# Performance work log

Measured on AMD Instinct MI355X. Metric: run time of the kernel, lower is better.

Reference implementation:

```python
import jax, jax.numpy as jnp
import numpy as np

N = 50000   # nodes
E = 800000  # edges
IN, H, O, C = 128, 256, 256, 64
G = 64      # graphs in batch


def setup_inputs() -> dict:
    key = jax.random.key(0)
    ks = jax.random.split(key, 10)
    x = jax.random.normal(ks[0], (N, IN), dtype=jnp.float32)
    edge_index = jax.random.randint(ks[1], (2, E), 0, N, dtype=jnp.int32)
    batch = jnp.sort(jax.random.randint(ks[2], (N,), 0, G, dtype=jnp.int32))
    # learned params (PyG GCNConv: weight [in, out] + bias [out]; nn.Linear)
    W1 = jax.random.normal(ks[3], (IN, H), dtype=jnp.float32) / np.sqrt(IN)
    b1 = jnp.zeros((H,), dtype=jnp.float32)
    W2 = jax.random.normal(ks[4], (H, O), dtype=jnp.float32) / np.sqrt(H)
    b2 = jnp.zeros((O,), dtype=jnp.float32)
    Wfc = jax.random.normal(ks[5], (O, C), dtype=jnp.float32) / np.sqrt(O)
    bfc = jnp.zeros((C,), dtype=jnp.float32)
    return {"x": x, "edge_index": edge_index, "batch": batch,
            "W1": W1, "b1": b1, "W2": W2, "b2": b2, "Wfc": Wfc, "bfc": bfc}


def reference(x, edge_index, batch, W1, b1, W2, b2, Wfc, bfc):
    src, dst = edge_index[0], edge_index[1]
    # degree with self-loops (PyG GCNConv default: add_self_loops=True, sym norm)
    deg = jax.ops.segment_sum(jnp.ones((E,), x.dtype), dst, num_segments=N) + 1.0
    dinv = jax.lax.rsqrt(deg)                      # D^{-1/2}
    edge_norm = (dinv[src] * dinv[dst])[:, None]   # [E, 1]
    self_norm = (dinv * dinv)[:, None]             # [N, 1] self-loop weight

    def gcn_conv(h, W, b):
        h = h @ W                                  # transform first (PyG order)
        agg = jax.ops.segment_sum(h[src] * edge_norm, dst, num_segments=N)
        return agg + h * self_norm + b

    h = jax.nn.gelu(gcn_conv(x, W1, b1), approximate=False)  # nn.GELU exact
    h = gcn_conv(h, W2, b2)

    # global_mean_pool over graph ids
    cnt = jax.ops.segment_sum(jnp.ones((N,), h.dtype), batch, num_segments=G)
    pooled = jax.ops.segment_sum(h, batch, num_segments=G) / jnp.maximum(cnt, 1.0)[:, None]
    return pooled @ Wfc + bfc                      # [G, C]
```

## Files before the change

### kernel.cpp

```cpp
#include <hip/hip_runtime.h>
#include <hip/hip_bf16.h>
#include <hip/hip_fp16.h>
#include <math.h>

#define NNODES 50000
#define NEDGES 800000
#define FIN 128
#define FH 256
#define NG 64
#define NC 64
#define SCAN_NB ((NNODES + 255) / 256)
#define NP 50176
#define QSK 196
#define DEG_BLOCKS ((NEDGES + 255) / 256)
#define SPLITX_ITEMS (NNODES * FIN / 4)
#define SPLITX_BLOCKS ((SPLITX_ITEMS + 255) / 256)
#define GEMM_MB ((NNODES + 127) / 128)
#define GEMM_BLKS (GEMM_MB * 2)
#define QTR (NP / 4)

#define NBUCK 196
#define BCAP 5120
#define BIN_CHUNK 4096
#define BIN_BLOCKS ((NEDGES + BIN_CHUNK - 1) / BIN_CHUNK)

typedef unsigned short bhalf;
typedef __attribute__((ext_vector_type(8))) short bf16x8;
typedef __attribute__((ext_vector_type(4))) float f32x4;
typedef __attribute__((ext_vector_type(4))) unsigned short u16x4;

__device__ inline bhalf f2bf_rn(float f) {
    unsigned int u = __float_as_uint(f);
    u += 0x7FFFu + ((u >> 16) & 1u);
    return (bhalf)(u >> 16);
}
__device__ inline float bf2f(bhalf h) { return __uint_as_float(((unsigned int)h) << 16); }
__device__ inline float2 bfpair(unsigned int u) {
    return make_float2(__uint_as_float(u << 16), __uint_as_float(u & 0xFFFF0000u));
}


__global__ void degree_splitx_kernel(const int* __restrict__ dst, int* __restrict__ degi,
                                     const float* __restrict__ x, bhalf* __restrict__ xb) {
    int b = blockIdx.x;
    if (b < DEG_BLOCKS) {
        int e = b * 256 + threadIdx.x;
        if (e < NEDGES) atomicAdd(&degi[dst[e]], 1);
    } else {
        int i = (b - DEG_BLOCKS) * 256 + threadIdx.x;
        if (i < SPLITX_ITEMS) {
            float4 v = *reinterpret_cast<const float4*>(&x[i * 4]);
            u16x4 o = {f2bf_rn(v.x), f2bf_rn(v.y), f2bf_rn(v.z), f2bf_rn(v.w)};
            *reinterpret_cast<u16x4*>(&xb[i * 4]) = o;
        }
    }
}


__global__ __launch_bounds__(256)
void scan_block_kernel(const int* __restrict__ degi, int* __restrict__ local_ex,
                       int* __restrict__ partial, float* __restrict__ dinv, int Nn) {
    __shared__ int s[256];
    int i = blockIdx.x * 256 + threadIdx.x;
    int v = (i < Nn) ? degi[i] : 0;
    s[threadIdx.x] = v;
    __syncthreads();
#pragma unroll
    for (int off = 1; off < 256; off <<= 1) {
        int t = (threadIdx.x >= off) ? s[threadIdx.x - off] : 0;
        __syncthreads();
        s[threadIdx.x] += t;
        __syncthreads();
    }
    if (i < Nn) {
        local_ex[i] = s[threadIdx.x] - v;
        dinv[i] = rsqrtf((float)v + 1.0f);
    }
    if (threadIdx.x == 255) partial[blockIdx.x] = s[255];
}


__global__ __launch_bounds__(256)
void add_offsets_kernel(int* __restrict__ row_start, const int* __restrict__ local_ex,
                        const int* __restrict__ partial, int* __restrict__ bcur,
                        const float* __restrict__ W1, bhalf* __restrict__ w1t, int Nn) {
    __shared__ int s[256];
    int t = threadIdx.x;
    s[t] = (t < blockIdx.x) ? partial[t] : 0;
    __syncthreads();
#pragma unroll
    for (int off = 128; off > 0; off >>= 1) {
        if (t < off) s[t] += s[t + off];
        __syncthreads();
    }
    int prefix = s[0];
    int i = blockIdx.x * 256 + t;
    if (i < Nn) row_start[i] = local_ex[i] + prefix;
    if (blockIdx.x == 0 && t < NBUCK) bcur[t] = t * BCAP;
    if (i < FIN * 256) {
        int k = i >> 8, n = i & 255;
        w1t[n * FIN + k] = f2bf_rn(W1[i]);
    }
}


__global__ __launch_bounds__(256)
void bin_kernel(const int* __restrict__ src, const int* __restrict__ dst,
                const float* __restrict__ dinv, int* __restrict__ bcur,
                uint2* __restrict__ binned) {
    __shared__ int hist[NBUCK];
    __shared__ int base[NBUCK];
    __shared__ int gb[NBUCK];
    __shared__ int lcur[NBUCK];
    __shared__ int scan_tmp[256];
    __shared__ uint2 stage[BIN_CHUNK];
    __shared__ unsigned char bid[BIN_CHUNK];
    int t = threadIdx.x;
    int e0 = blockIdx.x * BIN_CHUNK;
    for (int i = t; i < NBUCK; i += 256) hist[i] = 0;
    __syncthreads();
#pragma unroll
    for (int k = 0; k < BIN_CHUNK / 256; k++) {
        int e = e0 + k * 256 + t;
        if (e < NEDGES) atomicAdd(&hist[dst[e] >> 8], 1);
    }
    __syncthreads();
    int v = (t < NBUCK) ? hist[t] : 0;
    scan_tmp[t] = v;
    __syncthreads();
#pragma unroll
    for (int off = 1; off < 256; off <<= 1) {
        int x = (t >= off) ? scan_tmp[t - off] : 0;
        __syncthreads();
        scan_tmp[t] += x;
        __syncthreads();
    }
    if (t < NBUCK) {
        int ex = scan_tmp[t] - v;
        base[t] = ex;
        lcur[t] = ex;
        gb[t] = (v > 0) ? atomicAdd(&bcur[t], v) : 0;
    }
    __syncthreads();
#pragma unroll
    for (int k = 0; k < BIN_CHUNK / 256; k++) {
        int e = e0 + k * 256 + t;
        if (e < NEDGES) {
            int s = src[e], d = dst[e];
            int b = d >> 8;
            float nm = dinv[s] * dinv[d];
            int lp = atomicAdd(&lcur[b], 1);
            stage[lp] = make_uint2((unsigned int)s | ((unsigned int)(d & 255) << 17),
                                   __float_as_uint(nm));
            bid[lp] = (unsigned char)b;
        }
    }
    __syncthreads();
    int total = base[NBUCK - 1] + hist[NBUCK - 1];
    for (int i = t; i < total; i += 256) {
        int b = bid[i];
        binned[(size_t)gb[b] + (i - base[b])] = stage[i];
    }
}


__global__ __launch_bounds__(256)
void place_kernel(const uint2* __restrict__ binned, const int* __restrict__ bcur,
                  const int* __restrict__ row_start, uint2* __restrict__ edata) {
    __shared__ int lcur[256];
    int b = blockIdx.x;
    int t = threadIdx.x;
    lcur[t] = 0;
    __syncthreads();
    int cnt = bcur[b] - b * BCAP;
    int nb0 = b << 8;
    const uint2* bp = &binned[(size_t)b * BCAP];
    for (int i = t; i < cnt; i += 256) {
        uint2 e = bp[i];
        int dl = (e.x >> 17) & 255;
        int pos = row_start[nb0 + dl] + atomicAdd(&lcur[dl], 1);
        edata[pos] = make_uint2(e.x & 0x1FFFFu, e.y);
    }
}


__global__ __launch_bounds__(256)
void gather128_kernel(const bhalf* __restrict__ xb, const uint2* __restrict__ edata,
                      const int* __restrict__ row_start, const int* __restrict__ degi,
                      const float* __restrict__ dinv, bhalf* __restrict__ z, int Nn) {
    int node = blockIdx.x * 4 + (threadIdx.x >> 6);
    if (node >= Nn) return;
    int lane = threadIdx.x & 63;
    int st = row_start[node];
    int cnt = degi[node];
    float ax = 0.0f, ay = 0.0f;
    int j = 0;
    for (; j + 3 < cnt; j += 4) {
        uint2 e0 = edata[st + j],     e1 = edata[st + j + 1];
        uint2 e2 = edata[st + j + 2], e3 = edata[st + j + 3];
        float2 v0 = bfpair(*reinterpret_cast<const unsigned int*>(&xb[(size_t)e0.x * FIN + lane * 2]));
        float2 v1 = bfpair(*reinterpret_cast<const unsigned int*>(&xb[(size_t)e1.x * FIN + lane * 2]));
        float2 v2 = bfpair(*reinterpret_cast<const unsigned int*>(&xb[(size_t)e2.x * FIN + lane * 2]));
        float2 v3 = bfpair(*reinterpret_cast<const unsigned int*>(&xb[(size_t)e3.x * FIN + lane * 2]));
        float n0 = __uint_as_float(e0.y), n1 = __uint_as_float(e1.y);
        float n2 = __uint_as_float(e2.y), n3 = __uint_as_float(e3.y);
        ax += v0.x * n0 + v1.x * n1 + v2.x * n2 + v3.x * n3;
        ay += v0.y * n0 + v1.y * n1 + v2.y * n2 + v3.y * n3;
    }
    for (; j < cnt; j++) {
        uint2 e0 = edata[st + j];
        float2 v0 = bfpair(*reinterpret_cast<const unsigned int*>(&xb[(size_t)e0.x * FIN + lane * 2]));
        float n0 = __uint_as_float(e0.y);
        ax += v0.x * n0; ay += v0.y * n0;
    }
    float sn = dinv[node];
    sn *= sn;
    float2 xv = bfpair(*reinterpret_cast<const unsigned int*>(&xb[(size_t)node * FIN + lane * 2]));
    ushort2 o = {f2bf_rn(ax + xv.x * sn), f2bf_rn(ay + xv.y * sn)};
    *reinterpret_cast<ushort2*>(&z[(size_t)node * FIN + lane * 2]) = o;
}


__global__ __launch_bounds__(256)
void wt_build_kernel(const uint2* __restrict__ edata, const int* __restrict__ row_start,
                     const int* __restrict__ batch, const float* __restrict__ dinv,
                     bhalf* __restrict__ wthi, bhalf* __restrict__ wtlo) {
    __shared__ float acc[QTR];
    int g = blockIdx.x >> 2;
    int q = blockIdx.x & 3;
    int base = q * QTR;
    for (int i = threadIdx.x; i < QTR; i += 256) acc[i] = 0.0f;
    int lo = 0, hi = NNODES;
    while (lo < hi) { int m = (lo + hi) >> 1; if (batch[m] < g) lo = m + 1; else hi = m; }
    int na = lo;
    hi = NNODES;
    while (lo < hi) { int m = (lo + hi) >> 1; if (batch[m] < g + 1) lo = m + 1; else hi = m; }
    int nb = lo;
    int pa = (na < NNODES) ? row_start[na] : NEDGES;
    int pb = (nb < NNODES) ? row_start[nb] : NEDGES;
    __syncthreads();
    for (int p = pa + threadIdx.x; p < pb; p += 256) {
        uint2 e = edata[p];
        int s = (int)e.x - base;
        if ((unsigned int)s < (unsigned int)QTR)
            atomicAdd(&acc[s], __uint_as_float(e.y));
    }
    __syncthreads();
    size_t rowo = (size_t)g * NP + base;
    for (int i = threadIdx.x; i < QTR; i += 256) {
        int s = base + i;
        float v = acc[i];
        if (s >= na && s < nb) { float dv = dinv[s]; v += dv * dv; }
        bhalf hb = f2bf_rn(v);
        wthi[rowo + i] = hb;
        wtlo[rowo + i] = f2bf_rn(v - bf2f(hb));
    }
}


__global__ __launch_bounds__(256)
void gemm_kernel(const bhalf* __restrict__ A, const bhalf* __restrict__ Bt,
                 const float* __restrict__ bias, bhalf* __restrict__ h1t, int M, int Kp) {
    __shared__ bhalf As[128 * 72];
    __shared__ bhalf Bs[128 * 72];
    const int tid  = threadIdx.x;
    const int lane = tid & 63;
    const int wave = tid >> 6;
    const int quad = lane >> 4;
    const int l15  = lane & 15;
    const int wm = (wave & 1) * 64;
    const int wn = (wave >> 1) * 64;
    const int bm = (blockIdx.x >> 1) * 128;
    const int bn = (blockIdx.x & 1) * 128;

    f32x4 acc[4][4] = {};

    for (int k0 = 0; k0 < Kp; k0 += 64) {
#pragma unroll
        for (int i = 0; i < 4; i++) {
            int chunk = tid + i * 256;
            int r = chunk >> 3, c16 = chunk & 7;
            int gm = bm + r;
            float4 va = make_float4(0.f, 0.f, 0.f, 0.f);
            if (gm < M) va = *reinterpret_cast<const float4*>(&A[(size_t)gm * Kp + k0 + c16 * 8]);
            *reinterpret_cast<float4*>(&As[r * 72 + c16 * 8]) = va;
            float4 vb = *reinterpret_cast<const float4*>(&Bt[(size_t)(bn + r) * Kp + k0 + c16 * 8]);
            *reinterpret_cast<float4*>(&Bs[r * 72 + c16 * 8]) = vb;
        }
        __syncthreads();
#pragma unroll
        for (int kk = 0; kk < 64; kk += 32) {
            bf16x8 af[4], bfr[4];
#pragma unroll
            for (int mi = 0; mi < 4; mi++)
                af[mi] = *reinterpret_cast<const bf16x8*>(&As[(wm + mi * 16 + l15) * 72 + kk + quad * 8]);
#pragma unroll
            for (int ni = 0; ni < 4; ni++)
                bfr[ni] = *reinterpret_cast<const bf16x8*>(&Bs[(wn + ni * 16 + l15) * 72 + kk + quad * 8]);
#pragma unroll
            for (int mi = 0; mi < 4; mi++)
#pragma unroll
                for (int ni = 0; ni < 4; ni++)
                    acc[mi][ni] = __builtin_amdgcn_mfma_f32_16x16x32_bf16(af[mi], bfr[ni], acc[mi][ni], 0, 0, 0);
        }
        __syncthreads();
    }

#pragma unroll
    for (int mi = 0; mi < 4; mi++) {
        int row0 = bm + wm + mi * 16 + quad * 4;
#pragma unroll
        for (int ni = 0; ni < 4; ni++) {
            int col = bn + wn + ni * 16 + l15;
            float bv = bias[col];
            u16x4 o;
#pragma unroll
            for (int r = 0; r < 4; r++) {
                float v = acc[mi][ni][r] + bv;
                v = 0.5f * v * (1.0f + erff(v * 0.70710678118654752f));
                o[r] = f2bf_rn(v);
            }
            *reinterpret_cast<u16x4*>(&h1t[(size_t)col * NP + row0]) = o;
        }
    }
}


__global__ __launch_bounds__(256)
void qsum_mfma_kernel(const bhalf* __restrict__ h1t, const bhalf* __restrict__ wthi,
                      const bhalf* __restrict__ wtlo, float* __restrict__ qpart) {
    const int tid  = threadIdx.x;
    const int lane = tid & 63;
    const int wave = tid >> 6;
    const int quad = lane >> 4;
    const int l15  = lane & 15;
    const int m0 = wave * 64;
    const size_t kbase = (size_t)blockIdx.x * 256 + quad * 8;
    f32x4 acc[4][4] = {};
#pragma unroll
    for (int ks = 0; ks < 8; ks++) {
        size_t k0 = kbase + ks * 32;
        bf16x8 af[4], bh[4], bl[4];
#pragma unroll
        for (int mi = 0; mi < 4; mi++)
            af[mi] = *reinterpret_cast<const bf16x8*>(&h1t[(size_t)(m0 + mi * 16 + l15) * NP + k0]);
#pragma unroll
        for (int ni = 0; ni < 4; ni++) {
            bh[ni] = *reinterpret_cast<const bf16x8*>(&wthi[(size_t)(ni * 16 + l15) * NP + k0]);
            bl[ni] = *reinterpret_cast<const bf16x8*>(&wtlo[(size_t)(ni * 16 + l15) * NP + k0]);
        }
#pragma unroll
        for (int mi = 0; mi < 4; mi++)
#pragma unroll
            for (int ni = 0; ni < 4; ni++) {
                acc[mi][ni] = __builtin_amdgcn_mfma_f32_16x16x32_bf16(af[mi], bh[ni], acc[mi][ni], 0, 0, 0);
                acc[mi][ni] = __builtin_amdgcn_mfma_f32_16x16x32_bf16(af[mi], bl[ni], acc[mi][ni], 0, 0, 0);
            }
    }
    float* qp = &qpart[(size_t)blockIdx.x * NG * FH];
#pragma unroll
    for (int mi = 0; mi < 4; mi++) {
        int row0 = m0 + mi * 16 + quad * 4;
#pragma unroll
        for (int ni = 0; ni < 4; ni++) {
            int col = ni * 16 + l15;
            f32x4 o = {acc[mi][ni][0], acc[mi][ni][1], acc[mi][ni][2], acc[mi][ni][3]};
            *reinterpret_cast<f32x4*>(&qp[(size_t)col * FH + row0]) = o;
        }
    }
}


__global__ __launch_bounds__(256)
void p2fc_kernel(const float* __restrict__ qpart, const float* __restrict__ W2,
                 const float* __restrict__ b2, const int* __restrict__ batch,
                 const float* __restrict__ Wfc, const float* __restrict__ bfc,
                 float* __restrict__ out) {
    __shared__ float qg[FH];
    __shared__ float ps[FH];
    int g = blockIdx.x;
    int t = threadIdx.x;
    float s = 0.0f;
    for (int b = 0; b < QSK; b++)
        s += qpart[(size_t)b * NG * FH + (size_t)g * FH + t];
    qg[t] = s;
    int lo = 0, hi = NNODES;
    while (lo < hi) { int m = (lo + hi) >> 1; if (batch[m] < g) lo = m + 1; else hi = m; }
    int a = lo;
    lo = 0; hi = NNODES;
    while (lo < hi) { int m = (lo + hi) >> 1; if (batch[m] < g + 1) lo = m + 1; else hi = m; }
    float inv = 1.0f / fmaxf((float)(lo - a), 1.0f);
    __syncthreads();
    float acc = 0.0f;
    for (int k = 0; k < FH; k++)
        acc += qg[k] * W2[k * FH + t];
    ps[t] = acc * inv + b2[t];
    __syncthreads();
    if (t < NC) {
        float a2 = 0.0f;
        for (int cc = 0; cc < FH; cc++)
            a2 += ps[cc] * Wfc[cc * NC + t];
        out[g * NC + t] = a2 + bfc[t];
    }
}


extern "C" void kernel_launch(void* const* d_in, const int* in_sizes, int n_in,
                              void* d_out, int out_size, void* d_ws, size_t ws_size,
                              hipStream_t stream) {
    const float* x    = (const float*)d_in[0];
    const int*   ei   = (const int*)d_in[1];
    const int*   batch= (const int*)d_in[2];
    const float* W1   = (const float*)d_in[3];
    const float* b1   = (const float*)d_in[4];
    const float* W2   = (const float*)d_in[5];
    const float* b2   = (const float*)d_in[6];
    const float* Wfc  = (const float*)d_in[7];
    const float* bfc  = (const float*)d_in[8];
    float* out = (float*)d_out;

    const int* src = ei;
    const int* dst = ei + NEDGES;

    bhalf* xb        = (bhalf*)d_ws;
    bhalf* zb        = xb + (size_t)NNODES * FIN;
    bhalf* h1t       = zb + (size_t)NNODES * FIN;
    uint2* edata     = (uint2*)(h1t + (size_t)FH * NP);
    uint2* binned    = edata + NEDGES;
    int*   row_start = (int*)(binned + (size_t)NBUCK * BCAP);
    int*   local_ex  = row_start + NNODES;
    int*   partial   = local_ex + NNODES;
    int*   bcur      = partial + 256;
    float* dinv      = (float*)(bcur + 256);
    bhalf* w1t       = (bhalf*)(dinv + NNODES);
    bhalf* wthi      = w1t + 256 * FIN;
    bhalf* wtlo      = wthi + (size_t)NG * NP;
    float* qpart     = (float*)(wtlo + (size_t)NG * NP);
    int*   degi      = (int*)(qpart + (size_t)QSK * NG * FH);

    (void)hipMemsetAsync(degi, 0, (size_t)NNODES * 4, stream);

    degree_splitx_kernel<<<DEG_BLOCKS + SPLITX_BLOCKS, 256, 0, stream>>>(dst, degi, x, xb);
    scan_block_kernel<<<SCAN_NB, 256, 0, stream>>>(degi, local_ex, partial, dinv, NNODES);
    add_offsets_kernel<<<SCAN_NB, 256, 0, stream>>>(row_start, local_ex, partial, bcur,
                                                    W1, w1t, NNODES);
    bin_kernel<<<BIN_BLOCKS, 256, 0, stream>>>(src, dst, dinv, bcur, binned);
    place_kernel<<<NBUCK, 256, 0, stream>>>(binned, bcur, row_start, edata);

    gather128_kernel<<<(NNODES + 3) / 4, 256, 0, stream>>>(xb, edata, row_start, degi,
                                                           dinv, zb, NNODES);
    wt_build_kernel<<<NG * 4, 256, 0, stream>>>(edata, row_start, batch, dinv, wthi, wtlo);
    gemm_kernel<<<GEMM_BLKS, 256, 0, stream>>>(zb, w1t, b1, h1t, NNODES, FIN);

    qsum_mfma_kernel<<<QSK, 256, 0, stream>>>(h1t, wthi, wtlo, qpart);
    p2fc_kernel<<<NG, FH, 0, stream>>>(qpart, W2, b2, batch, Wfc, bfc, out);
}
```

Measured before the change: 294.5 us.

## Fold degree counting and CSR scan into bucket placement with packed 32-bit edges

Removes the separate atomic degree pass, the two scan kernels and the memset. Each place block now derives per-node degrees, dinv and row offsets from its binned bucket, working in shared memory. Edges are packed into 32 bits: a 16-bit source index plus a half-precision dinv of the destination, replacing the 8-byte (src, float norm) pairs. The gather factors the normalization as dinv[dst]*(sum dinv[src]*x + dinv[dst]*x), reading dinv per source. This cuts launches and edge bandwidth. It relies on node indices fitting in 16 bits, which fails for N=50000 > 65535? No, 50000 fits. It also introduces fp16 rounding of the norm weights in wt_build.

```diff
diff --git a/kernel.cpp b/kernel.cpp
--- a/kernel.cpp
+++ b/kernel.cpp
@@ -9,19 +9,18 @@
 #define FH 256
 #define NG 64
 #define NC 64
-#define SCAN_NB ((NNODES + 255) / 256)
 #define NP 50176
 #define QSK 196
-#define DEG_BLOCKS ((NEDGES + 255) / 256)
 #define SPLITX_ITEMS (NNODES * FIN / 4)
 #define SPLITX_BLOCKS ((SPLITX_ITEMS + 255) / 256)
+#define W1T_BLOCKS (FIN * 256 / 256)
 #define GEMM_MB ((NNODES + 127) / 128)
 #define GEMM_BLKS (GEMM_MB * 2)
 #define QTR (NP / 4)
 
 #define NBUCK 196
 #define BCAP 5120
-#define BIN_CHUNK 4096
+#define BIN_CHUNK 2048
 #define BIN_BLOCKS ((NEDGES + BIN_CHUNK - 1) / BIN_CHUNK)
 
 typedef unsigned short bhalf;
@@ -40,80 +39,36 @@
 }
 
 
-__global__ void degree_splitx_kernel(const int* __restrict__ dst, int* __restrict__ degi,
-                                     const float* __restrict__ x, bhalf* __restrict__ xb) {
+__global__ void splitx_kernel(const float* __restrict__ x, bhalf* __restrict__ xb,
+                              const float* __restrict__ W1, bhalf* __restrict__ w1t,
+                              int* __restrict__ bcur) {
     int b = blockIdx.x;
-    if (b < DEG_BLOCKS) {
-        int e = b * 256 + threadIdx.x;
-        if (e < NEDGES) atomicAdd(&degi[dst[e]], 1);
-    } else {
-        int i = (b - DEG_BLOCKS) * 256 + threadIdx.x;
+    if (b < SPLITX_BLOCKS) {
+        int i = b * 256 + threadIdx.x;
         if (i < SPLITX_ITEMS) {
             float4 v = *reinterpret_cast<const float4*>(&x[i * 4]);
             u16x4 o = {f2bf_rn(v.x), f2bf_rn(v.y), f2bf_rn(v.z), f2bf_rn(v.w)};
             *reinterpret_cast<u16x4*>(&xb[i * 4]) = o;
         }
-    }
-}
-
-
-__global__ __launch_bounds__(256)
-void scan_block_kernel(const int* __restrict__ degi, int* __restrict__ local_ex,
-                       int* __restrict__ partial, float* __restrict__ dinv, int Nn) {
-    __shared__ int s[256];
-    int i = blockIdx.x * 256 + threadIdx.x;
-    int v = (i < Nn) ? degi[i] : 0;
-    s[threadIdx.x] = v;
-    __syncthreads();
-#pragma unroll
-    for (int off = 1; off < 256; off <<= 1) {
-        int t = (threadIdx.x >= off) ? s[threadIdx.x - off] : 0;
-        __syncthreads();
-        s[threadIdx.x] += t;
-        __syncthreads();
-    }
-    if (i < Nn) {
-        local_ex[i] = s[threadIdx.x] - v;
-        dinv[i] = rsqrtf((float)v + 1.0f);
-    }
-    if (threadIdx.x == 255) partial[blockIdx.x] = s[255];
-}
-
-
-__global__ __launch_bounds__(256)
-void add_offsets_kernel(int* __restrict__ row_start, const int* __restrict__ local_ex,
-                        const int* __restrict__ partial, int* __restrict__ bcur,
-                        const float* __restrict__ W1, bhalf* __restrict__ w1t, int Nn) {
-    __shared__ int s[256];
-    int t = threadIdx.x;
-    s[t] = (t < blockIdx.x) ? partial[t] : 0;
-    __syncthreads();
-#pragma unroll
-    for (int off = 128; off > 0; off >>= 1) {
-        if (t < off) s[t] += s[t + off];
-        __syncthreads();
-    }
-    int prefix = s[0];
-    int i = blockIdx.x * 256 + t;
-    if (i < Nn) row_start[i] = local_ex[i] + prefix;
-    if (blockIdx.x == 0 && t < NBUCK) bcur[t] = t * BCAP;
-    if (i < FIN * 256) {
+    } else if (b < SPLITX_BLOCKS + W1T_BLOCKS) {
+        int i = (b - SPLITX_BLOCKS) * 256 + threadIdx.x;
         int k = i >> 8, n = i & 255;
         w1t[n * FIN + k] = f2bf_rn(W1[i]);
+    } else {
+        if (threadIdx.x < NBUCK) bcur[threadIdx.x] = threadIdx.x * BCAP;
     }
 }
 
 
 __global__ __launch_bounds__(256)
 void bin_kernel(const int* __restrict__ src, const int* __restrict__ dst,
-                const float* __restrict__ dinv, int* __restrict__ bcur,
-                uint2* __restrict__ binned) {
+                int* __restrict__ bcur, unsigned int* __restrict__ binned) {
     __shared__ int hist[NBUCK];
     __shared__ int base[NBUCK];
     __shared__ int gb[NBUCK];
     __shared__ int lcur[NBUCK];
     __shared__ int scan_tmp[256];
-    __shared__ uint2 stage[BIN_CHUNK];
+    __shared__ unsigned int stage[BIN_CHUNK];
     __shared__ unsigned char bid[BIN_CHUNK];
     int t = threadIdx.x;
     int e0 = blockIdx.x * BIN_CHUNK;
@@ -148,10 +103,8 @@
         if (e < NEDGES) {
             int s = src[e], d = dst[e];
             int b = d >> 8;
-            float nm = dinv[s] * dinv[d];
             int lp = atomicAdd(&lcur[b], 1);
-            stage[lp] = make_uint2((unsigned int)s | ((unsigned int)(d & 255) << 17),
-                                   __float_as_uint(nm));
+            stage[lp] = (unsigned int)s | ((unsigned int)(d & 255) << 16);
             bid[lp] = (unsigned char)b;
         }
     }
@@ -165,64 +118,103 @@
 
 
 __global__ __launch_bounds__(256)
-void place_kernel(const uint2* __restrict__ binned, const int* __restrict__ bcur,
-                  const int* __restrict__ row_start, uint2* __restrict__ edata) {
+void place_kernel(const unsigned int* __restrict__ binned, const int* __restrict__ bcur,
+                  int* __restrict__ row_start, float* __restrict__ dinv,
+                  unsigned int* __restrict__ edata) {
+    __shared__ unsigned int stage[BCAP];
+    __shared__ int sc[256];
+    __shared__ int deg[256];
+    __shared__ int lex[256];
     __shared__ int lcur[256];
-    int b = blockIdx.x;
-    int t = threadIdx.x;
+    __shared__ unsigned short dih[256];
+    __shared__ int s_ebase, s_cnt;
+    int b = blockIdx.x, t = threadIdx.x;
+    int c = (t < NBUCK) ? (bcur[t] - t * BCAP) : 0;
+    sc[t] = c;
+    __syncthreads();
+#pragma unroll
+    for (int off = 1; off < 256; off <<= 1) {
+        int x = (t >= off) ? sc[t - off] : 0;
+        __syncthreads();
+        sc[t] += x;
+        __syncthreads();
+    }
+    if (t == b) { s_ebase = sc[t] - c; s_cnt = c; }
+    deg[t] = 0;
+    __syncthreads();
+    int cnt = s_cnt, eb = s_ebase;
+    const unsigned int* bp = &binned[(size_t)b * BCAP];
+    for (int i = t; i < cnt; i += 256) stage[i] = bp[i];
+    __syncthreads();
+    for (int i = t; i < cnt; i += 256) atomicAdd(&deg[(stage[i] >> 16) & 255], 1);
+    __syncthreads();
+    int d = deg[t];
+    float di = rsqrtf((float)d + 1.0f);
+    int gn = (b << 8) + t;
+    if (gn < NNODES) dinv[gn] = di;
+    dih[t] = __half_as_ushort(__float2half(di));
+    sc[t] = d;
+    __syncthreads();
+#pragma unroll
+    for (int off = 1; off < 256; off <<= 1) {
+        int x = (t >= off) ? sc[t - off] : 0;
+        __syncthreads();
+        sc[t] += x;
+        __syncthreads();
+    }
+    int lexv = sc[t] - d;
+    lex[t] = lexv;
     lcur[t] = 0;
-    __syncthreads();
-    int cnt = bcur[b] - b * BCAP;
-    int nb0 = b << 8;
-    const uint2* bp = &binned[(size_t)b * BCAP];
+    if (gn <= NNODES) row_start[gn] = eb + lexv;
+    __syncthreads();
     for (int i = t; i < cnt; i += 256) {
-        uint2 e = bp[i];
-        int dl = (e.x >> 17) & 255;
-        int pos = row_start[nb0 + dl] + atomicAdd(&lcur[dl], 1);
-        edata[pos] = make_uint2(e.x & 0x1FFFFu, e.y);
-    }
-}
-
-
-__global__ __launch_bounds__(256)
-void gather128_kernel(const bhalf* __restrict__ xb, const uint2* __restrict__ edata,
-                      const int* __restrict__ row_start, const int* __restrict__ degi,
-                      const float* __restrict__ dinv, bhalf* __restrict__ z, int Nn) {
+        unsigned int e = stage[i];
+        int dl = (e >> 16) & 255;
+        int pos = eb + lex[dl] + atomicAdd(&lcur[dl], 1);
+        edata[pos] = (e & 0xFFFFu) | ((unsigned int)dih[dl] << 16);
+    }
+}
+
+
+__global__ __launch_bounds__(256)
+void gather128_kernel(const bhalf* __restrict__ xb, const unsigned int* __restrict__ edata,
+                      const int* __restrict__ row_start, const float* __restrict__ dinv,
+                      bhalf* __restrict__ z, int Nn) {
     int node = blockIdx.x * 4 + (threadIdx.x >> 6);
     if (node >= Nn) return;
     int lane = threadIdx.x & 63;
     int st = row_start[node];
-    int cnt = degi[node];
+    int cnt = row_start[node + 1] - st;
     float ax = 0.0f, ay = 0.0f;
     int j = 0;
     for (; j + 3 < cnt; j += 4) {
-        uint2 e0 = edata[st + j],     e1 = edata[st + j + 1];
-        uint2 e2 = edata[st + j + 2], e3 = edata[st + j + 3];
-        float2 v0 = bfpair(*reinterpret_cast<const unsigned int*>(&xb[(size_t)e0.x * FIN + lane * 2]));
-        float2 v1 = bfpair(*reinterpret_cast<const unsigned int*>(&xb[(size_t)e1.x * FIN + lane * 2]));
-        float2 v2 = bfpair(*reinterpret_cast<const unsigned int*>(&xb[(size_t)e2.x * FIN + lane * 2]));
-        float2 v3 = bfpair(*reinterpret_cast<const unsigned int*>(&xb[(size_t)e3.x * FIN + lane * 2]));
-        float n0 = __uint_as_float(e0.y), n1 = __uint_as_float(e1.y);
-        float n2 = __uint_as_float(e2.y), n3 = __uint_as_float(e3.y);
+        unsigned int e0 = edata[st + j],     e1 = edata[st + j + 1];
+        unsigned int e2 = edata[st + j + 2], e3 = edata[st + j + 3];
+        int s0 = e0 & 0xFFFFu, s1 = e1 & 0xFFFFu, s2 = e2 & 0xFFFFu, s3 = e3 & 0xFFFFu;
+        float2 v0 = bfpair(*reinterpret_cast<const unsigned int*>(&xb[(size_t)s0 * FIN + lane * 2]));
+        float2 v1 = bfpair(*reinterpret_cast<const unsigned int*>(&xb[(size_t)s1 * FIN + lane * 2]));
+        float2 v2 = bfpair(*reinterpret_cast<const unsigned int*>(&xb[(size_t)s2 * FIN + lane * 2]));
+        float2 v3 = bfpair(*reinterpret_cast<const unsigned int*>(&xb[(size_t)s3 * FIN + lane * 2]));
+        float n0 = dinv[s0], n1 = dinv[s1], n2 = dinv[s2], n3 = dinv[s3];
         ax += v0.x * n0 + v1.x * n1 + v2.x * n2 + v3.x * n3;
         ay += v0.y * n0 + v1.y * n1 + v2.y * n2 + v3.y * n3;
     }
     for (; j < cnt; j++) {
-        uint2 e0 = edata[st + j];
-        float2 v0 = bfpair(*reinterpret_cast<const unsigned int*>(&xb[(size_t)e0.x * FIN + lane * 2]));
-        float n0 = __uint_as_float(e0.y);
+        unsigned int e0 = edata[st + j];
+        int s0 = e0 & 0xFFFFu;
+        float2 v0 = bfpair(*reinterpret_cast<const unsigned int*>(&xb[(size_t)s0 * FIN + lane * 2]));
+        float n0 = dinv[s0];
         ax += v0.x * n0; ay += v0.y * n0;
     }
-    float sn = dinv[node];
-    sn *= sn;
+    float dn = dinv[node];
     float2 xv = bfpair(*reinterpret_cast<const unsigned int*>(&xb[(size_t)node * FIN + lane * 2]));
-    ushort2 o = {f2bf_rn(ax + xv.x * sn), f2bf_rn(ay + xv.y * sn)};
+    ushort2 o = {f2bf_rn(dn * (ax + xv.x * dn)), f2bf_rn(dn * (ay + xv.y * dn))};
     *reinterpret_cast<ushort2*>(&z[(size_t)node * FIN + lane * 2]) = o;
 }
 
 
 __global__ __launch_bounds__(256)
-void wt_build_kernel(const uint2* __restrict__ edata, const int* __restrict__ row_start,
+void wt_build_kernel(const unsigned int* __restrict__ edata, const int* __restrict__ row_start,
                      const int* __restrict__ batch, const float* __restrict__ dinv,
                      bhalf* __restrict__ wthi, bhalf* __restrict__ wtlo) {
     __shared__ float acc[QTR];
@@ -236,21 +228,23 @@
     hi = NNODES;
     while (lo < hi) { int m = (lo + hi) >> 1; if (batch[m] < g + 1) lo = m + 1; else hi = m; }
     int nb = lo;
-    int pa = (na < NNODES) ? row_start[na] : NEDGES;
-    int pb = (nb < NNODES) ? row_start[nb] : NEDGES;
+    int pa = row_start[na];
+    int pb = row_start[nb];
     __syncthreads();
     for (int p = pa + threadIdx.x; p < pb; p += 256) {
-        uint2 e = edata[p];
-        int s = (int)e.x - base;
+        unsigned int e = edata[p];
+        int s = (int)(e & 0xFFFFu) - base;
         if ((unsigned int)s < (unsigned int)QTR)
-            atomicAdd(&acc[s], __uint_as_float(e.y));
+            atomicAdd(&acc[s], __half2float(__ushort_as_half((unsigned short)(e >> 16))));
     }
     __syncthreads();
     size_t rowo = (size_t)g * NP + base;
     for (int i = threadIdx.x; i < QTR; i += 256) {
         int s = base + i;
+        float dv = (s < NNODES) ? dinv[s] : 0.0f;
         float v = acc[i];
-        if (s >= na && s < nb) { float dv = dinv[s]; v += dv * dv; }
+        if (s >= na && s < nb) v += dv;
+        v *= dv;
         bhalf hb = f2bf_rn(v);
         wthi[rowo + i] = hb;
         wtlo[rowo + i] = f2bf_rn(v - bf2f(hb));
@@ -425,30 +419,22 @@
     bhalf* xb        = (bhalf*)d_ws;
     bhalf* zb        = xb + (size_t)NNODES * FIN;
     bhalf* h1t       = zb + (size_t)NNODES * FIN;
-    uint2* edata     = (uint2*)(h1t + (size_t)FH * NP);
-    uint2* binned    = edata + NEDGES;
+    unsigned int* edata  = (unsigned int*)(h1t + (size_t)FH * NP);
+    unsigned int* binned = edata + NEDGES;
     int*   row_start = (int*)(binned + (size_t)NBUCK * BCAP);
-    int*   local_ex  = row_start + NNODES;
-    int*   partial   = local_ex + NNODES;
-    int*   bcur      = partial + 256;
+    int*   bcur      = row_start + NNODES + 256;
     float* dinv      = (float*)(bcur + 256);
-    bhalf* w1t       = (bhalf*)(dinv + NNODES);
+    bhalf* w1t       = (bhalf*)(dinv + NNODES + 256);
     bhalf* wthi      = w1t + 256 * FIN;
     bhalf* wtlo      = wthi + (size_t)NG * NP;
     float* qpart     = (float*)(wtlo + (size_t)NG * NP);
-    int*   degi      = (int*)(qpart + (size_t)QSK * NG * FH);
-
-    (void)hipMemsetAsync(degi, 0, (size_t)NNODES * 4, stream);
-
-    degree_splitx_kernel<<<DEG_BLOCKS + SPLITX_BLOCKS, 256, 0, stream>>>(dst, degi, x, xb);
-    scan_block_kernel<<<SCAN_NB, 256, 0, stream>>>(degi, local_ex, partial, dinv, NNODES);
-    add_offsets_kernel<<<SCAN_NB, 256, 0, stream>>>(row_start, local_ex, partial, bcur,
-                                                    W1, w1t, NNODES);
-    bin_kernel<<<BIN_BLOCKS, 256, 0, stream>>>(src, dst, dinv, bcur, binned);
-    place_kernel<<<NBUCK, 256, 0, stream>>>(binned, bcur, row_start, edata);
-
-    gather128_kernel<<<(NNODES + 3) / 4, 256, 0, stream>>>(xb, edata, row_start, degi,
-                                                           dinv, zb, NNODES);
+
+    splitx_kernel<<<SPLITX_BLOCKS + W1T_BLOCKS + 1, 256, 0, stream>>>(x, xb, W1, w1t, bcur);
+    bin_kernel<<<BIN_BLOCKS, 256, 0, stream>>>(src, dst, bcur, binned);
+    place_kernel<<<NBUCK, 256, 0, stream>>>(binned, bcur, row_start, dinv, edata);
+
+    gather128_kernel<<<(NNODES + 3) / 4, 256, 0, stream>>>(xb, edata, row_start, dinv,
+                                                           zb, NNODES);
     wt_build_kernel<<<NG * 4, 256, 0, stream>>>(edata, row_start, batch, dinv, wthi, wtlo);
     gemm_kernel<<<GEMM_BLKS, 256, 0, stream>>>(zb, w1t, b1, h1t, NNODES, FIN);
 
```

Measured after the change: 246.8 us. 16.2% less time.
